# Kernel optimization log

Hardware: AMD Instinct MI355X
Metric: run time of the kernel (lower is better)

Reference implementation:

```python
import jax, jax.numpy as jnp
import numpy as np

DM, NE, ES, ESZ = 1024, 16, 4, 64  # dm, nexperts, expertsets, expertsize (dff = NE*ES*ESZ = 4096)
BATCH, SEQ = 8, 2048


def setup_inputs() -> dict:
    key = jax.random.key(0)
    k = jax.random.split(key, 5)
    scale = 0.02
    return {
        "x": jax.random.normal(k[0], (BATCH, SEQ, DM), dtype=jnp.float32),
        "controller": jax.random.normal(k[1], (DM, NE, ES), dtype=jnp.float32) * scale,
        "f1": jax.random.normal(k[2], (DM, NE, ES, ESZ), dtype=jnp.float32) * scale,
        "f2": jax.random.normal(k[3], (NE, ES, ESZ, DM), dtype=jnp.float32) * scale,
        "bias": jax.random.normal(k[4], (NE, ES, ESZ), dtype=jnp.float32) * scale,
    }


def reference(x, controller, f1, f2, bias):
    ne = controller.shape[1]
    d = x.shape[-1]
    # group tokens: [..., (b t), d] -> [..., b, t, d] with t = nexperts
    grouped = x.reshape(x.shape[:-2] + (-1, ne, d))
    # controller logits per token/expert/expertset: [..., b, t, e, s]
    logits = jnp.einsum('...btd,des->...btes', grouped, controller)
    # deterministic tiebreaker over the token-within-group axis t
    tie = jnp.linspace(0.0, 1e-6, ne, dtype=logits.dtype).reshape(ne, 1, 1)
    logits = logits + tie
    # hard top-1 permutation: for each (e, s) pick the argmax token t (one-hot over t)
    perm = (logits == jnp.max(logits, axis=-3, keepdims=True)).astype(x.dtype)
    # dispatch: select the chosen token's activations per (e, s): [..., b, e, s, d]
    sel = jnp.einsum('...btd,...btes->...besd', grouped, perm)
    # expert FFN up-projection + bias + relu: [..., b, e, s, f]
    inner = jax.nn.relu(jnp.einsum('...besd,desf->...besf', sel, f1) + bias)
    # expert FFN down-projection: [..., b, e, s, d]
    inter = jnp.einsum('...besf,esfd->...besd', inner, f2)
    # un-permute back to token positions: [..., b, t, d]
    out = jnp.einsum('...besd,...btes->...btd', inter, perm)
    return out.reshape(x.shape)
```

## Files before the change

kernel.cpp:

```cpp
#include <hip/hip_runtime.h>

#define DM   1024
#define NES  64
#define ESZ  64
#define NG   1024
#define TOK  16

typedef __bf16 bf16;
typedef __bf16 bf16x4 __attribute__((ext_vector_type(4)));
typedef __bf16 bf16x8 __attribute__((ext_vector_type(8)));
typedef float  f32x4  __attribute__((ext_vector_type(4)));

__global__ __launch_bounds__(256) void k0_transpose(const float* __restrict__ f1,
                                                    const float* __restrict__ f2,
                                                    bf16* __restrict__ f1p,
                                                    bf16* __restrict__ f2t) {
    __shared__ float tile[64 * 65];
    const int es = blockIdx.y, d0 = blockIdx.x * 64, tid = threadIdx.x;
    #pragma unroll
    for (int i = 0; i < 4; ++i) {
        int idx = i * 256 + tid; int r = idx >> 4, c4 = (idx & 15) * 4;
        float4 v = *(const float4*)(f1 + (size_t)(d0 + r) * 4096 + es * 64 + c4);
        tile[r * 65 + c4] = v.x; tile[r * 65 + c4 + 1] = v.y;
        tile[r * 65 + c4 + 2] = v.z; tile[r * 65 + c4 + 3] = v.w;
    }
    __syncthreads();
    #pragma unroll
    for (int i = 0; i < 2; ++i) {
        int idx = i * 256 + tid; int f = idx >> 3, dl0 = (idx & 7) * 8;
        bf16x8 o;
        #pragma unroll
        for (int j = 0; j < 8; ++j) o[j] = (bf16)tile[(dl0 + j) * 65 + f];
        *(bf16x8*)(f1p + (size_t)es * 65536 + f * 1024 + d0 + dl0) = o;
    }
    __syncthreads();
    #pragma unroll
    for (int i = 0; i < 4; ++i) {
        int idx = i * 256 + tid; int r = idx >> 4, c4 = (idx & 15) * 4;
        float4 v = *(const float4*)(f2 + (size_t)es * 65536 + r * 1024 + d0 + c4);
        tile[r * 65 + c4] = v.x; tile[r * 65 + c4 + 1] = v.y;
        tile[r * 65 + c4 + 2] = v.z; tile[r * 65 + c4 + 3] = v.w;
    }
    __syncthreads();
    #pragma unroll
    for (int i = 0; i < 2; ++i) {
        int idx = i * 256 + tid; int dl = idx >> 3, f0 = (idx & 7) * 8;
        bf16x8 o;
        #pragma unroll
        for (int j = 0; j < 8; ++j) o[j] = (bf16)tile[(f0 + j) * 65 + dl];
        *(bf16x8*)(f2t + (size_t)es * 65536 + (size_t)(d0 + dl) * 64 + f0) = o;
    }
}

__global__ __launch_bounds__(256) void k1_logits(const float* __restrict__ x,
                                                 const float* __restrict__ ctrl,
                                                 int* __restrict__ sel) {
    __shared__ __align__(16) float xs[TOK * 128];
    __shared__ float sl[TOK * NES];
    const int bg  = blockIdx.x;
    const int tid = threadIdx.x;
    const int es  = tid & 63;
    const int tq  = tid >> 6;
    const float* xg = x + (size_t)bg * (TOK * DM);
    float acc[4] = {0.f, 0.f, 0.f, 0.f};
    for (int d0 = 0; d0 < DM; d0 += 128) {
        __syncthreads();
        #pragma unroll
        for (int c = 0; c < 2; ++c) {
            int idx = tid + c * 256;
            int tr  = idx >> 5;
            int c4  = idx & 31;
            float4 v = *(const float4*)(xg + tr * DM + d0 + c4 * 4);
            *(float4*)(xs + tr * 128 + c4 * 4) = v;
        }
        __syncthreads();
        for (int dl = 0; dl < 128; ++dl) {
            float c = ctrl[(d0 + dl) * 64 + es];
            #pragma unroll
            for (int i = 0; i < 4; ++i)
                acc[i] += xs[(tq * 4 + i) * 128 + dl] * c;
        }
    }
    #pragma unroll
    for (int i = 0; i < 4; ++i) {
        int t = tq * 4 + i;
        sl[t * NES + es] = acc[i] + (float)t * (1e-6f / 15.f);
    }
    __syncthreads();
    if (tid < NES) {
        float best = -1e30f; int bi = 0;
        #pragma unroll
        for (int t = 0; t < TOK; ++t) {
            float v = sl[t * NES + tid];
            if (v >= best) { best = v; bi = t; }
        }
        sel[bg * NES + tid] = bi;
    }
}

__global__ __launch_bounds__(256) void k2_ffn1(const float* __restrict__ x,
                                               const bf16* __restrict__ f1p,
                                               const float* __restrict__ bias,
                                               const int* __restrict__ sel,
                                               bf16* __restrict__ inner) {
    __shared__ int  sel_s[128];
    __shared__ __align__(16) bf16 As[128 * 40];
    __shared__ __align__(16) bf16 Bs[64 * 40];
    const int es  = blockIdx.y;
    const int g0  = blockIdx.x * 128;
    const int tid = threadIdx.x;
    if (tid < 128) sel_s[tid] = sel[(g0 + tid) * 64 + es];
    __syncthreads();

    const int w = tid >> 6, l = tid & 63, quad = l >> 4, lr = l & 15;
    int tokrow[4];
    #pragma unroll
    for (int p = 0; p < 4; ++p) {
        int grow = p * 32 + (tid >> 3);
        tokrow[p] = (g0 + grow) * 16 + sel_s[grow];
    }
    const int c4 = (tid & 7) * 4;
    const int bf = tid >> 2, bd = (tid & 3) * 8;
    const bf16* f1es = f1p + (size_t)es * (DM * ESZ);

    f32x4 acc[2][4];
    #pragma unroll
    for (int mt = 0; mt < 2; ++mt)
        #pragma unroll
        for (int nt = 0; nt < 4; ++nt)
            acc[mt][nt] = (f32x4){0.f, 0.f, 0.f, 0.f};

    for (int k0 = 0; k0 < DM; k0 += 32) {
        #pragma unroll
        for (int p = 0; p < 4; ++p) {
            int grow = p * 32 + (tid >> 3);
            float4 v = *(const float4*)(x + (size_t)tokrow[p] * DM + k0 + c4);
            bf16x4 ob = {(bf16)v.x, (bf16)v.y, (bf16)v.z, (bf16)v.w};
            *(bf16x4*)(As + grow * 40 + c4) = ob;
        }
        {
            bf16x8 v = *(const bf16x8*)(f1es + bf * 1024 + k0 + bd);
            *(bf16x8*)(Bs + bf * 40 + bd) = v;
        }
        __syncthreads();
        bf16x8 av[2], bv[4];
        #pragma unroll
        for (int mt = 0; mt < 2; ++mt)
            av[mt] = *(const bf16x8*)(As + (w * 32 + mt * 16 + lr) * 40 + quad * 8);
        #pragma unroll
        for (int nt = 0; nt < 4; ++nt)
            bv[nt] = *(const bf16x8*)(Bs + (nt * 16 + lr) * 40 + quad * 8);
        #pragma unroll
        for (int mt = 0; mt < 2; ++mt)
            #pragma unroll
            for (int nt = 0; nt < 4; ++nt)
                acc[mt][nt] = __builtin_amdgcn_mfma_f32_16x16x32_bf16(
                    av[mt], bv[nt], acc[mt][nt], 0, 0, 0);
        __syncthreads();
    }
    bf16* innes = inner + (size_t)es * (NG * ESZ);
    #pragma unroll
    for (int mt = 0; mt < 2; ++mt)
        #pragma unroll
        for (int nt = 0; nt < 4; ++nt) {
            int f = nt * 16 + lr;
            float b = bias[es * 64 + f];
            #pragma unroll
            for (int r = 0; r < 4; ++r) {
                int grow = w * 32 + mt * 16 + quad * 4 + r;
                float v = acc[mt][nt][r] + b;
                v = v > 0.f ? v : 0.f;
                innes[(size_t)(g0 + grow) * 64 + f] = (bf16)v;
            }
        }
}

__global__ __launch_bounds__(256) void k3_ffn2(const bf16* __restrict__ inner,
                                               const bf16* __restrict__ f2t,
                                               const int* __restrict__ sel,
                                               float* __restrict__ out) {
    __shared__ float accs[512 * 32];
    const int d0  = blockIdx.x * 32;
    const int g0  = blockIdx.y * 32;
    const int tid = threadIdx.x;
    #pragma unroll
    for (int i = 0; i < 16; ++i)
        ((float4*)accs)[i * 256 + tid] = (float4){0.f, 0.f, 0.f, 0.f};

    const int w = tid >> 6, l = tid & 63, quad = l >> 4, lr = l & 15;
    const int mh = w >> 1, nh = w & 1;
    const bf16* pa = inner + (size_t)(g0 + mh * 16 + lr) * 64 + quad * 8;
    const bf16* pb = f2t   + (size_t)(d0 + nh * 16 + lr) * 64 + quad * 8;
    const int*  ps = sel + (g0 + mh * 16 + quad * 4) * 64;

    bf16x8 a0 = *(const bf16x8*)(pa);
    bf16x8 a1 = *(const bf16x8*)(pa + 32);
    bf16x8 b0 = *(const bf16x8*)(pb);
    bf16x8 b1 = *(const bf16x8*)(pb + 32);
    int t0 = ps[0], t1 = ps[64], t2 = ps[128], t3 = ps[192];
    __syncthreads();

    for (int es = 0; es < NES; ++es) {
        int e2 = es + 1 < NES ? es + 1 : NES - 1;
        const bf16* qa = pa + (size_t)e2 * 65536;
        const bf16* qb = pb + (size_t)e2 * 65536;
        bf16x8 na0 = *(const bf16x8*)(qa);
        bf16x8 na1 = *(const bf16x8*)(qa + 32);
        bf16x8 nb0 = *(const bf16x8*)(qb);
        bf16x8 nb1 = *(const bf16x8*)(qb + 32);
        int nt0 = ps[e2], nt1 = ps[64 + e2], nt2 = ps[128 + e2], nt3 = ps[192 + e2];

        f32x4 acc = {0.f, 0.f, 0.f, 0.f};
        acc = __builtin_amdgcn_mfma_f32_16x16x32_bf16(a0, b0, acc, 0, 0, 0);
        acc = __builtin_amdgcn_mfma_f32_16x16x32_bf16(a1, b1, acc, 0, 0, 0);
        int tt[4] = {t0, t1, t2, t3};
        #pragma unroll
        for (int r = 0; r < 4; ++r) {
            int gl   = mh * 16 + quad * 4 + r;
            int t    = tt[r];
            int row  = gl * 16 + t;
            int col  = nh * 16 + lr;
            int scol = col ^ ((t & 7) << 2);
            accs[row * 32 + scol] += acc[r];
        }
        a0 = na0; a1 = na1; b0 = nb0; b1 = nb1;
        t0 = nt0; t1 = nt1; t2 = nt2; t3 = nt3;
    }
    __syncthreads();
    #pragma unroll
    for (int i = 0; i < 16; ++i) {
        int fi = i * 256 + tid;
        int row = fi >> 3, q = fi & 7;
        int scol4 = (q * 4) ^ ((row & 7) << 2);
        float4 v = *(float4*)(accs + row * 32 + scol4);
        *(float4*)(out + (size_t)(g0 * 16 + row) * DM + d0 + q * 4) = v;
    }
}

extern "C" void kernel_launch(void* const* d_in, const int* in_sizes, int n_in,
                              void* d_out, int out_size, void* d_ws, size_t ws_size,
                              hipStream_t stream) {
    const float* x    = (const float*)d_in[0];
    const float* ctrl = (const float*)d_in[1];
    const float* f1   = (const float*)d_in[2];
    const float* f2   = (const float*)d_in[3];
    const float* bias = (const float*)d_in[4];
    float* out = (float*)d_out;

    char* ws = (char*)d_ws;
    bf16* f1p   = (bf16*)(ws);
    bf16* f2t   = (bf16*)(ws + 8388608);
    bf16* inner = (bf16*)(ws + 16777216);
    int*  sel   = (int*)(ws + 25165824);

    hipLaunchKernelGGL(k0_transpose, dim3(16, 64), dim3(256), 0, stream, f1, f2, f1p, f2t);
    hipLaunchKernelGGL(k1_logits,    dim3(1024),   dim3(256), 0, stream, x, ctrl, sel);
    hipLaunchKernelGGL(k2_ffn1,      dim3(8, 64),  dim3(256), 0, stream, x, f1p, bias, sel, inner);
    hipLaunchKernelGGL(k3_ffn2,      dim3(32, 32), dim3(256), 0, stream, inner, f2t, sel, out);
}
```

Baseline: 357.1 us.

## Split ffn2 expert-set loop across waves with packed selections and LDS atomics

k3_ffn2 now gives each wave 16 of the 64 expert-sets and a full 32x32 output tile, where before each wave owned a 16x16 quadrant and looped over all 64. Partial products are scattered into shared memory with atomicAdd, and token indices come from a packed 4-bit-per-entry array that k1 now also writes. k1_logits drops the LDS staging of x and uses 128 threads, each reading x directly with 8 tokens per thread. This trades serial loop length and scalar index loads for LDS atomic contention and higher register use.

```diff
diff --git a/kernel.cpp b/kernel.cpp
--- a/kernel.cpp
+++ b/kernel.cpp
@@ -52,38 +52,33 @@
     }
 }
 
-__global__ __launch_bounds__(256) void k1_logits(const float* __restrict__ x,
+__global__ __launch_bounds__(128) void k1_logits(const float* __restrict__ x,
                                                  const float* __restrict__ ctrl,
-                                                 int* __restrict__ sel) {
-    __shared__ __align__(16) float xs[TOK * 128];
+                                                 int* __restrict__ sel,
+                                                 unsigned* __restrict__ selp) {
     __shared__ float sl[TOK * NES];
+    __shared__ int   st[NES];
     const int bg  = blockIdx.x;
     const int tid = threadIdx.x;
     const int es  = tid & 63;
-    const int tq  = tid >> 6;
-    const float* xg = x + (size_t)bg * (TOK * DM);
-    float acc[4] = {0.f, 0.f, 0.f, 0.f};
-    for (int d0 = 0; d0 < DM; d0 += 128) {
-        __syncthreads();
-        #pragma unroll
-        for (int c = 0; c < 2; ++c) {
-            int idx = tid + c * 256;
-            int tr  = idx >> 5;
-            int c4  = idx & 31;
-            float4 v = *(const float4*)(xg + tr * DM + d0 + c4 * 4);
-            *(float4*)(xs + tr * 128 + c4 * 4) = v;
-        }
-        __syncthreads();
-        for (int dl = 0; dl < 128; ++dl) {
-            float c = ctrl[(d0 + dl) * 64 + es];
-            #pragma unroll
-            for (int i = 0; i < 4; ++i)
-                acc[i] += xs[(tq * 4 + i) * 128 + dl] * c;
-        }
-    }
-    #pragma unroll
-    for (int i = 0; i < 4; ++i) {
-        int t = tq * 4 + i;
+    const int wq  = __builtin_amdgcn_readfirstlane(tid >> 6);
+    const float* xg = x + (size_t)bg * (TOK * DM) + (size_t)wq * 8 * DM;
+    const float* cp = ctrl + es;
+    float acc[8] = {0.f,0.f,0.f,0.f,0.f,0.f,0.f,0.f};
+    #pragma unroll 2
+    for (int dl = 0; dl < DM; dl += 4) {
+        float c0 = cp[(dl + 0) * 64], c1 = cp[(dl + 1) * 64],
+              c2 = cp[(dl + 2) * 64], c3 = cp[(dl + 3) * 64];
+        #pragma unroll
+        for (int i = 0; i < 8; ++i) {
+            const float* xr = xg + i * DM + dl;
+            acc[i] += xr[0] * c0; acc[i] += xr[1] * c1;
+            acc[i] += xr[2] * c2; acc[i] += xr[3] * c3;
+        }
+    }
+    #pragma unroll
+    for (int i = 0; i < 8; ++i) {
+        int t = wq * 8 + i;
         sl[t * NES + es] = acc[i] + (float)t * (1e-6f / 15.f);
     }
     __syncthreads();
@@ -95,6 +90,14 @@
             if (v >= best) { best = v; bi = t; }
         }
         sel[bg * NES + tid] = bi;
+        st[tid] = bi;
+    }
+    __syncthreads();
+    if (tid < 8) {
+        unsigned p = 0;
+        #pragma unroll
+        for (int k = 0; k < 8; ++k) p |= (unsigned)st[tid * 8 + k] << (4 * k);
+        selp[bg * 8 + tid] = p;
     }
 }
 
@@ -177,54 +180,85 @@
 
 __global__ __launch_bounds__(256) void k3_ffn2(const bf16* __restrict__ inner,
                                                const bf16* __restrict__ f2t,
-                                               const int* __restrict__ sel,
+                                               const unsigned* __restrict__ selp,
                                                float* __restrict__ out) {
     __shared__ float accs[512 * 32];
     const int d0  = blockIdx.x * 32;
     const int g0  = blockIdx.y * 32;
     const int tid = threadIdx.x;
+    const int w = tid >> 6, l = tid & 63, quad = l >> 4, lr = l & 15;
+
+    uint2 sp[2][4];
+    #pragma unroll
+    for (int mt = 0; mt < 2; ++mt)
+        #pragma unroll
+        for (int r = 0; r < 4; ++r) {
+            int gl = mt * 16 + quad * 4 + r;
+            sp[mt][r] = *(const uint2*)(selp + (size_t)(g0 + gl) * 8 + w * 2);
+        }
+
     #pragma unroll
     for (int i = 0; i < 16; ++i)
         ((float4*)accs)[i * 256 + tid] = (float4){0.f, 0.f, 0.f, 0.f};
 
-    const int w = tid >> 6, l = tid & 63, quad = l >> 4, lr = l & 15;
-    const int mh = w >> 1, nh = w & 1;
-    const bf16* pa = inner + (size_t)(g0 + mh * 16 + lr) * 64 + quad * 8;
-    const bf16* pb = f2t   + (size_t)(d0 + nh * 16 + lr) * 64 + quad * 8;
-    const int*  ps = sel + (g0 + mh * 16 + quad * 4) * 64;
-
-    bf16x8 a0 = *(const bf16x8*)(pa);
-    bf16x8 a1 = *(const bf16x8*)(pa + 32);
-    bf16x8 b0 = *(const bf16x8*)(pb);
-    bf16x8 b1 = *(const bf16x8*)(pb + 32);
-    int t0 = ps[0], t1 = ps[64], t2 = ps[128], t3 = ps[192];
-    __syncthreads();
-
-    for (int es = 0; es < NES; ++es) {
-        int e2 = es + 1 < NES ? es + 1 : NES - 1;
-        const bf16* qa = pa + (size_t)e2 * 65536;
-        const bf16* qb = pb + (size_t)e2 * 65536;
-        bf16x8 na0 = *(const bf16x8*)(qa);
-        bf16x8 na1 = *(const bf16x8*)(qa + 32);
-        bf16x8 nb0 = *(const bf16x8*)(qb);
-        bf16x8 nb1 = *(const bf16x8*)(qb + 32);
-        int nt0 = ps[e2], nt1 = ps[64 + e2], nt2 = ps[128 + e2], nt3 = ps[192 + e2];
-
-        f32x4 acc = {0.f, 0.f, 0.f, 0.f};
-        acc = __builtin_amdgcn_mfma_f32_16x16x32_bf16(a0, b0, acc, 0, 0, 0);
-        acc = __builtin_amdgcn_mfma_f32_16x16x32_bf16(a1, b1, acc, 0, 0, 0);
-        int tt[4] = {t0, t1, t2, t3};
-        #pragma unroll
-        for (int r = 0; r < 4; ++r) {
-            int gl   = mh * 16 + quad * 4 + r;
-            int t    = tt[r];
-            int row  = gl * 16 + t;
-            int col  = nh * 16 + lr;
-            int scol = col ^ ((t & 7) << 2);
-            accs[row * 32 + scol] += acc[r];
-        }
-        a0 = na0; a1 = na1; b0 = nb0; b1 = nb1;
-        t0 = nt0; t1 = nt1; t2 = nt2; t3 = nt3;
+    const size_t esoff = (size_t)(w * 16) * 65536;
+    const bf16* pa[2];
+    const bf16* pb[2];
+    pa[0] = inner + esoff + (size_t)(g0 + lr) * 64 + quad * 8;
+    pa[1] = pa[0] + 16 * 64;
+    pb[0] = f2t + esoff + (size_t)(d0 + lr) * 64 + quad * 8;
+    pb[1] = pb[0] + 16 * 64;
+
+    bf16x8 A[2][2], B[2][2];
+    #pragma unroll
+    for (int mt = 0; mt < 2; ++mt) {
+        A[mt][0] = *(const bf16x8*)(pa[mt]);
+        A[mt][1] = *(const bf16x8*)(pa[mt] + 32);
+        B[mt][0] = *(const bf16x8*)(pb[mt]);
+        B[mt][1] = *(const bf16x8*)(pb[mt] + 32);
+    }
+    __syncthreads();
+
+    #pragma unroll
+    for (int i = 0; i < 16; ++i) {
+        const int inext = (i < 15) ? i + 1 : 15;
+        bf16x8 An[2][2], Bn[2][2];
+        #pragma unroll
+        for (int mt = 0; mt < 2; ++mt) {
+            An[mt][0] = *(const bf16x8*)(pa[mt] + (size_t)inext * 65536);
+            An[mt][1] = *(const bf16x8*)(pa[mt] + (size_t)inext * 65536 + 32);
+            Bn[mt][0] = *(const bf16x8*)(pb[mt] + (size_t)inext * 65536);
+            Bn[mt][1] = *(const bf16x8*)(pb[mt] + (size_t)inext * 65536 + 32);
+        }
+        f32x4 acc[2][2];
+        #pragma unroll
+        for (int mt = 0; mt < 2; ++mt)
+            #pragma unroll
+            for (int nt = 0; nt < 2; ++nt) {
+                f32x4 z = {0.f, 0.f, 0.f, 0.f};
+                z = __builtin_amdgcn_mfma_f32_16x16x32_bf16(A[mt][0], B[nt][0], z, 0, 0, 0);
+                acc[mt][nt] = __builtin_amdgcn_mfma_f32_16x16x32_bf16(A[mt][1], B[nt][1], z, 0, 0, 0);
+            }
+        #pragma unroll
+        for (int mt = 0; mt < 2; ++mt)
+            #pragma unroll
+            for (int r = 0; r < 4; ++r) {
+                unsigned pw = (i < 8) ? sp[mt][r].x : sp[mt][r].y;
+                int t  = (pw >> ((i & 7) * 4)) & 15;
+                int gl = mt * 16 + quad * 4 + r;
+                int base = gl * 512 + t * 32;
+                int sw = (t & 7) << 2;
+                #pragma unroll
+                for (int nt = 0; nt < 2; ++nt) {
+                    int col = nt * 16 + lr;
+                    atomicAdd(&accs[base + (col ^ sw)], acc[mt][nt][r]);
+                }
+            }
+        #pragma unroll
+        for (int mt = 0; mt < 2; ++mt) {
+            A[mt][0] = An[mt][0]; A[mt][1] = An[mt][1];
+            B[mt][0] = Bn[mt][0]; B[mt][1] = Bn[mt][1];
+        }
     }
     __syncthreads();
     #pragma unroll
@@ -248,13 +282,14 @@
     float* out = (float*)d_out;
 
     char* ws = (char*)d_ws;
-    bf16* f1p   = (bf16*)(ws);
-    bf16* f2t   = (bf16*)(ws + 8388608);
-    bf16* inner = (bf16*)(ws + 16777216);
-    int*  sel   = (int*)(ws + 25165824);
+    bf16*     f1p   = (bf16*)(ws);
+    bf16*     f2t   = (bf16*)(ws + 8388608);
+    bf16*     inner = (bf16*)(ws + 16777216);
+    int*      sel   = (int*)(ws + 25165824);
+    unsigned* selp  = (unsigned*)(ws + 25427968);
 
     hipLaunchKernelGGL(k0_transpose, dim3(16, 64), dim3(256), 0, stream, f1, f2, f1p, f2t);
-    hipLaunchKernelGGL(k1_logits,    dim3(1024),   dim3(256), 0, stream, x, ctrl, sel);
+    hipLaunchKernelGGL(k1_logits,    dim3(1024),   dim3(128), 0, stream, x, ctrl, sel, selp);
     hipLaunchKernelGGL(k2_ffn1,      dim3(8, 64),  dim3(256), 0, stream, x, f1p, bias, sel, inner);
-    hipLaunchKernelGGL(k3_ffn2,      dim3(32, 32), dim3(256), 0, stream, inner, f2t, sel, out);
-}
+    hipLaunchKernelGGL(k3_ffn2,      dim3(32, 32), dim3(256), 0, stream, inner, f2t, selp, out);
+}
```

Measured after the change: 686.2 us. 92.2% more time.

## Deepen k3 prefetch, pack selection indices, vectorize logits LDS reads

Applied to the files above, without the earlier changes.

k3_ffn2 is fully unrolled over expert sets. It keeps a four-slot register ring that prefetches operands two steps ahead instead of one. The per-token selection indices are packed into 4-bit fields by k1 and loaded once per thread at kernel start, which removes the scattered sel loads from the inner loop. k1_logits reads x from LDS as float4 with a padded row stride and loads four controller values per step. The prefetch near the loop end reads past the valid expert-set range into adjacent workspace, and the extra live registers may lower occupancy.

```diff
diff --git a/kernel.cpp b/kernel.cpp
--- a/kernel.cpp
+++ b/kernel.cpp
@@ -54,14 +54,17 @@
 
 __global__ __launch_bounds__(256) void k1_logits(const float* __restrict__ x,
                                                  const float* __restrict__ ctrl,
-                                                 int* __restrict__ sel) {
-    __shared__ __align__(16) float xs[TOK * 128];
+                                                 int* __restrict__ sel,
+                                                 unsigned* __restrict__ selp) {
+    __shared__ __align__(16) float xs[TOK * 132];
     __shared__ float sl[TOK * NES];
+    __shared__ int   st[NES];
     const int bg  = blockIdx.x;
     const int tid = threadIdx.x;
     const int es  = tid & 63;
     const int tq  = tid >> 6;
     const float* xg = x + (size_t)bg * (TOK * DM);
+    const float* cp = ctrl + es;
     float acc[4] = {0.f, 0.f, 0.f, 0.f};
     for (int d0 = 0; d0 < DM; d0 += 128) {
         __syncthreads();
@@ -69,16 +72,29 @@
         for (int c = 0; c < 2; ++c) {
             int idx = tid + c * 256;
             int tr  = idx >> 5;
-            int c4  = idx & 31;
-            float4 v = *(const float4*)(xg + tr * DM + d0 + c4 * 4);
-            *(float4*)(xs + tr * 128 + c4 * 4) = v;
-        }
-        __syncthreads();
-        for (int dl = 0; dl < 128; ++dl) {
-            float c = ctrl[(d0 + dl) * 64 + es];
-            #pragma unroll
-            for (int i = 0; i < 4; ++i)
-                acc[i] += xs[(tq * 4 + i) * 128 + dl] * c;
+            int c4  = (idx & 31) * 4;
+            float4 v = *(const float4*)(xg + tr * DM + d0 + c4);
+            *(float4*)(xs + tr * 132 + c4) = v;
+        }
+        __syncthreads();
+        #pragma unroll 2
+        for (int dl4 = 0; dl4 < 128; dl4 += 4) {
+            float4 v0 = *(const float4*)(xs + (tq * 4 + 0) * 132 + dl4);
+            float4 v1 = *(const float4*)(xs + (tq * 4 + 1) * 132 + dl4);
+            float4 v2 = *(const float4*)(xs + (tq * 4 + 2) * 132 + dl4);
+            float4 v3 = *(const float4*)(xs + (tq * 4 + 3) * 132 + dl4);
+            float c0 = cp[(size_t)(d0 + dl4 + 0) * 64];
+            float c1 = cp[(size_t)(d0 + dl4 + 1) * 64];
+            float c2 = cp[(size_t)(d0 + dl4 + 2) * 64];
+            float c3 = cp[(size_t)(d0 + dl4 + 3) * 64];
+            acc[0] += v0.x * c0; acc[1] += v1.x * c0;
+            acc[2] += v2.x * c0; acc[3] += v3.x * c0;
+            acc[0] += v0.y * c1; acc[1] += v1.y * c1;
+            acc[2] += v2.y * c1; acc[3] += v3.y * c1;
+            acc[0] += v0.z * c2; acc[1] += v1.z * c2;
+            acc[2] += v2.z * c2; acc[3] += v3.z * c2;
+            acc[0] += v0.w * c3; acc[1] += v1.w * c3;
+            acc[2] += v2.w * c3; acc[3] += v3.w * c3;
         }
     }
     #pragma unroll
@@ -95,6 +111,14 @@
             if (v >= best) { best = v; bi = t; }
         }
         sel[bg * NES + tid] = bi;
+        st[tid] = bi;
+    }
+    __syncthreads();
+    if (tid < 8) {
+        unsigned p = 0;
+        #pragma unroll
+        for (int k = 0; k < 8; ++k) p |= (unsigned)st[tid * 8 + k] << (4 * k);
+        selp[bg * 8 + tid] = p;
     }
 }
 
@@ -177,54 +201,66 @@
 
 __global__ __launch_bounds__(256) void k3_ffn2(const bf16* __restrict__ inner,
                                                const bf16* __restrict__ f2t,
-                                               const int* __restrict__ sel,
+                                               const unsigned* __restrict__ selp,
                                                float* __restrict__ out) {
     __shared__ float accs[512 * 32];
     const int d0  = blockIdx.x * 32;
     const int g0  = blockIdx.y * 32;
     const int tid = threadIdx.x;
+    const int w = tid >> 6, l = tid & 63, quad = l >> 4, lr = l & 15;
+    const int mh = w >> 1, nh = w & 1;
+
+    unsigned sp[4][8];
+    #pragma unroll
+    for (int r = 0; r < 4; ++r) {
+        int gl = mh * 16 + quad * 4 + r;
+        uint4 a = *(const uint4*)(selp + (size_t)(g0 + gl) * 8);
+        uint4 b = *(const uint4*)(selp + (size_t)(g0 + gl) * 8 + 4);
+        sp[r][0] = a.x; sp[r][1] = a.y; sp[r][2] = a.z; sp[r][3] = a.w;
+        sp[r][4] = b.x; sp[r][5] = b.y; sp[r][6] = b.z; sp[r][7] = b.w;
+    }
     #pragma unroll
     for (int i = 0; i < 16; ++i)
         ((float4*)accs)[i * 256 + tid] = (float4){0.f, 0.f, 0.f, 0.f};
 
-    const int w = tid >> 6, l = tid & 63, quad = l >> 4, lr = l & 15;
-    const int mh = w >> 1, nh = w & 1;
     const bf16* pa = inner + (size_t)(g0 + mh * 16 + lr) * 64 + quad * 8;
     const bf16* pb = f2t   + (size_t)(d0 + nh * 16 + lr) * 64 + quad * 8;
-    const int*  ps = sel + (g0 + mh * 16 + quad * 4) * 64;
-
-    bf16x8 a0 = *(const bf16x8*)(pa);
-    bf16x8 a1 = *(const bf16x8*)(pa + 32);
-    bf16x8 b0 = *(const bf16x8*)(pb);
-    bf16x8 b1 = *(const bf16x8*)(pb + 32);
-    int t0 = ps[0], t1 = ps[64], t2 = ps[128], t3 = ps[192];
-    __syncthreads();
-
-    for (int es = 0; es < NES; ++es) {
-        int e2 = es + 1 < NES ? es + 1 : NES - 1;
-        const bf16* qa = pa + (size_t)e2 * 65536;
-        const bf16* qb = pb + (size_t)e2 * 65536;
-        bf16x8 na0 = *(const bf16x8*)(qa);
-        bf16x8 na1 = *(const bf16x8*)(qa + 32);
-        bf16x8 nb0 = *(const bf16x8*)(qb);
-        bf16x8 nb1 = *(const bf16x8*)(qb + 32);
-        int nt0 = ps[e2], nt1 = ps[64 + e2], nt2 = ps[128 + e2], nt3 = ps[192 + e2];
-
-        f32x4 acc = {0.f, 0.f, 0.f, 0.f};
-        acc = __builtin_amdgcn_mfma_f32_16x16x32_bf16(a0, b0, acc, 0, 0, 0);
-        acc = __builtin_amdgcn_mfma_f32_16x16x32_bf16(a1, b1, acc, 0, 0, 0);
-        int tt[4] = {t0, t1, t2, t3};
+
+    bf16x8 A[4][2], B[4][2];
+    #pragma unroll
+    for (int s = 0; s < 2; ++s) {
+        const bf16* qa = pa + (size_t)s * 65536;
+        const bf16* qb = pb + (size_t)s * 65536;
+        A[s][0] = *(const bf16x8*)(qa);
+        A[s][1] = *(const bf16x8*)(qa + 32);
+        B[s][0] = *(const bf16x8*)(qb);
+        B[s][1] = *(const bf16x8*)(qb + 32);
+    }
+    __syncthreads();
+
+    #pragma unroll
+    for (int es = 0; es < 64; ++es) {
+        const int lp = (es + 2) & 3;
+        const bf16* qa = pa + (size_t)(es + 2) * 65536;
+        const bf16* qb = pb + (size_t)(es + 2) * 65536;
+        A[lp][0] = *(const bf16x8*)(qa);
+        A[lp][1] = *(const bf16x8*)(qa + 32);
+        B[lp][0] = *(const bf16x8*)(qb);
+        B[lp][1] = *(const bf16x8*)(qb + 32);
+
+        const int s = es & 3;
+        f32x4 z = {0.f, 0.f, 0.f, 0.f};
+        z = __builtin_amdgcn_mfma_f32_16x16x32_bf16(A[s][0], B[s][0], z, 0, 0, 0);
+        z = __builtin_amdgcn_mfma_f32_16x16x32_bf16(A[s][1], B[s][1], z, 0, 0, 0);
+
+        const int dw = es >> 3, sh = (es & 7) * 4;
         #pragma unroll
         for (int r = 0; r < 4; ++r) {
+            int t    = (sp[r][dw] >> sh) & 15;
             int gl   = mh * 16 + quad * 4 + r;
-            int t    = tt[r];
-            int row  = gl * 16 + t;
-            int col  = nh * 16 + lr;
-            int scol = col ^ ((t & 7) << 2);
-            accs[row * 32 + scol] += acc[r];
-        }
-        a0 = na0; a1 = na1; b0 = nb0; b1 = nb1;
-        t0 = nt0; t1 = nt1; t2 = nt2; t3 = nt3;
+            int scol = (nh * 16 + lr) ^ ((t & 7) << 2);
+            accs[(gl * 16 + t) * 32 + scol] += z[r];
+        }
     }
     __syncthreads();
     #pragma unroll
@@ -248,13 +284,14 @@
     float* out = (float*)d_out;
 
     char* ws = (char*)d_ws;
-    bf16* f1p   = (bf16*)(ws);
-    bf16* f2t   = (bf16*)(ws + 8388608);
-    bf16* inner = (bf16*)(ws + 16777216);
-    int*  sel   = (int*)(ws + 25165824);
+    bf16*     f1p   = (bf16*)(ws);
+    bf16*     f2t   = (bf16*)(ws + 8388608);
+    bf16*     inner = (bf16*)(ws + 16777216);
+    int*      sel   = (int*)(ws + 25165824);
+    unsigned* selp  = (unsigned*)(ws + 25427968);
 
     hipLaunchKernelGGL(k0_transpose, dim3(16, 64), dim3(256), 0, stream, f1, f2, f1p, f2t);
-    hipLaunchKernelGGL(k1_logits,    dim3(1024),   dim3(256), 0, stream, x, ctrl, sel);
+    hipLaunchKernelGGL(k1_logits,    dim3(1024),   dim3(256), 0, stream, x, ctrl, sel, selp);
     hipLaunchKernelGGL(k2_ffn1,      dim3(8, 64),  dim3(256), 0, stream, x, f1p, bias, sel, inner);
-    hipLaunchKernelGGL(k3_ffn2,      dim3(32, 32), dim3(256), 0, stream, inner, f2t, sel, out);
-}
+    hipLaunchKernelGGL(k3_ffn2,      dim3(32, 32), dim3(256), 0, stream, inner, f2t, selp, out);
+}
```

Result: no change. 352.7 us (-1.2%).
